# Performance work log

Hardware: AMD Instinct MI355X
Metric: run time of the kernel (lower is better)

The kernel has to match this reference:

```python
import jax, jax.numpy as jnp
import numpy as np

N_NODES = 100000
N_EDGES = 20000
N_PAIRS = 640000
IN_CH = 128
HEADS = 4
OUT_CH = 32


def setup_inputs() -> dict:
    key = jax.random.key(0)
    k1, k2, k3, k4, k5 = jax.random.split(key, 5)
    X = jax.random.normal(k1, (N_NODES, IN_CH), dtype=jnp.float32)
    # nn.Linear(in, H*C, bias=False); stored as [in, H*C] so X0 = X @ W
    W = jax.random.normal(k2, (IN_CH, HEADS * OUT_CH), dtype=jnp.float32) * (1.0 / np.sqrt(IN_CH))
    stdv = (6.0 / (HEADS + OUT_CH)) ** 0.5
    att_e = jax.random.uniform(k3, (1, HEADS, OUT_CH), dtype=jnp.float32, minval=-stdv, maxval=stdv)
    vertex = jax.random.randint(k4, (N_PAIRS,), 0, N_NODES, dtype=jnp.int64)
    edges = jax.random.randint(k5, (N_PAIRS,), 0, N_EDGES, dtype=jnp.int64)
    return {"X": X, "W": W, "att_e": att_e, "vertex": vertex, "edges": edges}


def reference(X, W, att_e, vertex, edges):
    N = X.shape[0]
    H, C = HEADS, OUT_CH
    X0 = X @ W                                  # [N, H*C]
    Xv_hc = X0.reshape(N, H, C)
    Xve = Xv_hc[vertex]                          # [M, H, C] gather
    # scatter-mean over hyperedges
    esum = jax.ops.segment_sum(Xve, edges, num_segments=N_EDGES)
    ecnt = jax.ops.segment_sum(jnp.ones((Xve.shape[0],), X.dtype), edges, num_segments=N_EDGES)
    Xe = esum / jnp.maximum(ecnt, 1.0)[:, None, None]   # [E, H, C]
    alpha_e = (Xe * att_e).sum(-1)               # [E, H]
    a_ev = alpha_e[edges]                        # [M, H]
    alpha = jax.nn.leaky_relu(a_ev, 0.01)
    # per-vertex softmax over incident hyperedges
    amax = jax.ops.segment_max(alpha, vertex, num_segments=N)
    alpha = jnp.exp(alpha - amax[vertex])
    asum = jax.ops.segment_sum(alpha, vertex, num_segments=N)
    alpha = alpha / (asum[vertex] + 1e-8)
    Xev = Xe[edges] * alpha[:, :, None]          # [M, H, C]
    Xv = jax.ops.segment_sum(Xev, vertex, num_segments=N)
    return Xv.reshape(N, H * C) + X0
```

## Files before the change

### kernel.cpp

```cpp
#include <hip/hip_runtime.h>
#include <hip/hip_bf16.h>

#define N_NODES 100000
#define N_EDGES 20000
#define N_PAIRS 640000
#define CH 128
#define HEADS 4
#define MAXDV 32

#define NG_GEMM 1563
#define NR_RANK 2500
#define INTERLEAVE (2*NG_GEMM)

#define OFF_X0H   0UL
#define OFF_XEH   25600000UL
#define OFF_RANK  30720000UL
#define OFF_WT    33280000UL
#define OFF_ALPHA 33320000UL
#define OFF_OFFE  33640000UL
#define OFF_ENDE  33720000UL
#define OFF_OFFV  33800000UL
#define OFF_ENDV  34200000UL
#define OFF_PIDXE 34600000UL
#define OFF_PIDXV 37160000UL
#define OFF_CNTE  39720000UL
#define OFF_CNTV  39800000UL
#define OFF_TOT   40200000UL
#define ZERO_BYTES 480008UL

typedef __attribute__((ext_vector_type(8))) short bf16x8;
typedef __attribute__((ext_vector_type(4))) float f32x4;

__device__ inline short f2bf(float f) {
    __hip_bfloat16 h = __float2bfloat16(f);
    return reinterpret_cast<short&>(h);
}
__device__ inline float bf2f(short s) {
    unsigned int u = ((unsigned int)(unsigned short)s) << 16;
    union { unsigned int u; float f; } c; c.u = u;
    return c.f;
}

__global__ __launch_bounds__(256) void k_wprep(const float* __restrict__ W,
                                               short* __restrict__ Wt) {
    const int idx = blockIdx.x * 256 + threadIdx.x;
    const int n = idx >> 7, k = idx & 127;
    Wt[n * CH + k] = f2bf(W[k * CH + n]);
}

__device__ inline void gemm_body(int gb, const float* __restrict__ X,
                                 const short* __restrict__ Wt,
                                 short* __restrict__ X0h) {
    const int t = threadIdx.x;
    const int wave = t >> 6, lane = t & 63;
    const int r0 = gb * 64 + (wave >> 1) * 32;
    const int c0 = (wave & 1) * 64;
    const int lrow = lane & 15, lk8 = (lane >> 4) * 8;

    f32x4 acc[2][4] = {};

#pragma unroll
    for (int kk = 0; kk < 4; ++kk) {
        const int ks = kk * 32 + lk8;
        bf16x8 a[2], b[4];
#pragma unroll
        for (int m = 0; m < 2; ++m) {
            int row = r0 + m * 16 + lrow;
            row = min(row, N_NODES - 1);
            const float* p = &X[(size_t)row * CH + ks];
            const float4 x0 = *(const float4*)p;
            const float4 x1 = *(const float4*)(p + 4);
            a[m][0] = f2bf(x0.x); a[m][1] = f2bf(x0.y);
            a[m][2] = f2bf(x0.z); a[m][3] = f2bf(x0.w);
            a[m][4] = f2bf(x1.x); a[m][5] = f2bf(x1.y);
            a[m][6] = f2bf(x1.z); a[m][7] = f2bf(x1.w);
        }
#pragma unroll
        for (int n = 0; n < 4; ++n) {
            int col = c0 + n * 16 + lrow;
            b[n] = *(const bf16x8*)&Wt[col * CH + ks];
        }
#pragma unroll
        for (int m = 0; m < 2; ++m)
#pragma unroll
            for (int n = 0; n < 4; ++n)
                acc[m][n] = __builtin_amdgcn_mfma_f32_16x16x32_bf16(a[m], b[n], acc[m][n], 0, 0, 0);
    }

#pragma unroll
    for (int m = 0; m < 2; ++m) {
#pragma unroll
        for (int reg = 0; reg < 4; ++reg) {
            const int row = r0 + m * 16 + (lane >> 4) * 4 + reg;
            if (row < N_NODES) {
#pragma unroll
                for (int n = 0; n < 4; ++n)
                    X0h[(size_t)row * CH + c0 + n * 16 + (lane & 15)] = f2bf(acc[m][n][reg]);
            }
        }
    }
}

__device__ inline void rank_body(int rb, const int* __restrict__ vertex,
                                 const int* __restrict__ edges,
                                 int* __restrict__ cnt_e,
                                 int* __restrict__ cnt_v,
                                 unsigned int* __restrict__ rank_pack) {
    const int m = rb * 256 + threadIdx.x;
    const int e = edges[m];
    const int v = vertex[m];
    int re = atomicAdd(&cnt_e[e], 1);
    int rv = atomicAdd(&cnt_v[v], 1);
    rank_pack[m] = ((unsigned)rv << 16) | (unsigned)re;
}

__global__ __launch_bounds__(256) void k_gemm_rank(const float* __restrict__ X,
                                                   const short* __restrict__ Wt,
                                                   short* __restrict__ X0h,
                                                   const int* __restrict__ vertex,
                                                   const int* __restrict__ edges,
                                                   int* __restrict__ cnt_e,
                                                   int* __restrict__ cnt_v,
                                                   unsigned int* __restrict__ rank_pack) {
    const int bid = blockIdx.x;
    if (bid < INTERLEAVE) {
        if ((bid & 1) == 0) gemm_body(bid >> 1, X, Wt, X0h);
        else                rank_body(bid >> 1, vertex, edges, cnt_e, cnt_v, rank_pack);
    } else {
        rank_body(bid - INTERLEAVE + NG_GEMM, vertex, edges, cnt_e, cnt_v, rank_pack);
    }
}

__global__ __launch_bounds__(256) void k_offsets2(const int* __restrict__ cnt_e,
                                                  int* __restrict__ off_e,
                                                  int* __restrict__ end_e,
                                                  const int* __restrict__ cnt_v,
                                                  int* __restrict__ off_v,
                                                  int* __restrict__ end_v,
                                                  int* __restrict__ totals) {
    __shared__ int s[256];
    __shared__ int base;
    const int bid = blockIdx.x, t = threadIdx.x;
    const int* cnt; int* off; int* end; int* total; int n, i;
    if (bid < 79) { cnt = cnt_e; off = off_e; end = end_e; total = &totals[0]; n = N_EDGES;  i = bid * 256 + t; }
    else          { cnt = cnt_v; off = off_v; end = end_v; total = &totals[1]; n = N_NODES; i = (bid - 79) * 256 + t; }
    const int c = (i < n) ? cnt[i] : 0;
    s[t] = c;
    __syncthreads();
    for (int d = 1; d < 256; d <<= 1) {
        int x = (t >= d) ? s[t - d] : 0;
        __syncthreads();
        s[t] += x;
        __syncthreads();
    }
    if (t == 0) base = atomicAdd(total, s[255]);
    __syncthreads();
    if (i < n) {
        int o = base + s[t] - c;
        off[i] = o;
        end[i] = o + c;
    }
}

__global__ __launch_bounds__(256) void k_scatter(const int* __restrict__ vertex,
                                                 const int* __restrict__ edges,
                                                 const unsigned int* __restrict__ rank_pack,
                                                 const int* __restrict__ off_e,
                                                 const int* __restrict__ off_v,
                                                 int* __restrict__ vlist_e,
                                                 int* __restrict__ elist_v) {
    const int m = blockIdx.x * 256 + threadIdx.x;
    const int e = edges[m];
    const int v = vertex[m];
    const unsigned rp = rank_pack[m];
    vlist_e[off_e[e] + (int)(rp & 0xffffu)] = v;
    elist_v[off_v[v] + (int)(rp >> 16)] = e;
}

__global__ __launch_bounds__(256) void k_edge(const short* __restrict__ X0h,
                                              const int* __restrict__ off_e,
                                              const int* __restrict__ end_e,
                                              const int* __restrict__ vlist,
                                              const float* __restrict__ att,
                                              short* __restrict__ Xeh,
                                              float* __restrict__ alpha_le) {
    const int t = threadIdx.x;
    const int slot = t >> 5, lane = t & 31, h = lane >> 3;
    const int e = blockIdx.x * 8 + slot;
    const int s = off_e[e], en = end_e[e];
    const int deg = en - s;

    float4 acc = make_float4(0.f, 0.f, 0.f, 0.f);
    for (int c0 = 0; c0 < deg; c0 += 32) {
        const int cn = min(32, deg - c0);
        int vl = (lane < cn) ? vlist[s + c0 + lane] : 0;
#pragma unroll 4
        for (int j = 0; j < cn; ++j) {
            int vj = __shfl(vl, j, 32);
            short4 x = *(const short4*)&X0h[(size_t)vj * CH + (lane << 2)];
            acc.x += bf2f(x.x); acc.y += bf2f(x.y);
            acc.z += bf2f(x.z); acc.w += bf2f(x.w);
        }
    }
    const float invd = 1.0f / fmaxf((float)deg, 1.0f);
    float4 xe = make_float4(acc.x * invd, acc.y * invd, acc.z * invd, acc.w * invd);
    short4 xh;
    xh.x = f2bf(xe.x); xh.y = f2bf(xe.y); xh.z = f2bf(xe.z); xh.w = f2bf(xe.w);
    *(short4*)&Xeh[(size_t)e * CH + (lane << 2)] = xh;

    const float4 av = *(const float4*)&att[lane << 2];
    float p = xe.x * av.x + xe.y * av.y + xe.z * av.z + xe.w * av.w;
#pragma unroll
    for (int o = 4; o; o >>= 1) p += __shfl_xor(p, o);
    if ((lane & 7) == 0) {
        float a = p;
        alpha_le[e * HEADS + h] = (a > 0.f) ? a : 0.01f * a;
    }
}

__global__ __launch_bounds__(256) void k_vertex(const short* __restrict__ X0h,
                                                const short* __restrict__ Xeh,
                                                const float* __restrict__ alpha_le,
                                                const int* __restrict__ off_v,
                                                const int* __restrict__ end_v,
                                                const int* __restrict__ elist,
                                                float* __restrict__ out) {
    const int t = threadIdx.x;
    const int slot = t >> 5, lane = t & 31, h = lane >> 3;
    const int v = blockIdx.x * 8 + slot;
    const int s = off_v[v], en = end_v[v];
    const int deg = en - s;

    __shared__ int   se[8][MAXDV];
    __shared__ float sa[8][MAXDV * HEADS];

    if (deg <= MAXDV && lane < deg) {
        int e = elist[s + lane];
        se[slot][lane] = e;
        *(float4*)&sa[slot][lane << 2] = *(const float4*)&alpha_le[e * HEADS];
    }
    const short4 resh = *(const short4*)&X0h[(size_t)v * CH + (lane << 2)];
    __syncthreads();

    float4 acc = make_float4(0.f, 0.f, 0.f, 0.f);
    if (deg <= MAXDV) {
        float mx = -INFINITY;
        for (int j = 0; j < deg; ++j) mx = fmaxf(mx, sa[slot][(j << 2) + h]);
        float ssum = 0.f;
        for (int j = 0; j < deg; ++j) ssum += __expf(sa[slot][(j << 2) + h] - mx);
        const float inv = 1.0f / (ssum + 1e-8f);
        for (int j = 0; j < deg; ++j) {
            float w = __expf(sa[slot][(j << 2) + h] - mx) * inv;
            short4 x = *(const short4*)&Xeh[(size_t)se[slot][j] * CH + (lane << 2)];
            acc.x += w * bf2f(x.x); acc.y += w * bf2f(x.y);
            acc.z += w * bf2f(x.z); acc.w += w * bf2f(x.w);
        }
    } else {
        float mx = -INFINITY;
        for (int j = 0; j < deg; ++j) mx = fmaxf(mx, alpha_le[elist[s + j] * HEADS + h]);
        float ssum = 0.f;
        for (int j = 0; j < deg; ++j) ssum += __expf(alpha_le[elist[s + j] * HEADS + h] - mx);
        const float inv = 1.0f / (ssum + 1e-8f);
        for (int j = 0; j < deg; ++j) {
            int e = elist[s + j];
            float w = __expf(alpha_le[e * HEADS + h] - mx) * inv;
            short4 x = *(const short4*)&Xeh[(size_t)e * CH + (lane << 2)];
            acc.x += w * bf2f(x.x); acc.y += w * bf2f(x.y);
            acc.z += w * bf2f(x.z); acc.w += w * bf2f(x.w);
        }
    }
    float4 o = make_float4(acc.x + bf2f(resh.x), acc.y + bf2f(resh.y),
                           acc.z + bf2f(resh.z), acc.w + bf2f(resh.w));
    ((float4*)out)[(size_t)v * 32 + lane] = o;
}

extern "C" void kernel_launch(void* const* d_in, const int* in_sizes, int n_in,
                              void* d_out, int out_size, void* d_ws, size_t ws_size,
                              hipStream_t stream) {
    const float* X      = (const float*)d_in[0];
    const float* W      = (const float*)d_in[1];
    const float* att    = (const float*)d_in[2];
    const int*   vertex = (const int*)d_in[3];
    const int*   edges  = (const int*)d_in[4];
    float* out = (float*)d_out;

    char* ws = (char*)d_ws;
    short* X0h      = (short*)(ws + OFF_X0H);
    short* Xeh      = (short*)(ws + OFF_XEH);
    unsigned int* rank_pack = (unsigned int*)(ws + OFF_RANK);
    short* Wt       = (short*)(ws + OFF_WT);
    float* alpha_le = (float*)(ws + OFF_ALPHA);
    int* off_e   = (int*)(ws + OFF_OFFE);
    int* end_e   = (int*)(ws + OFF_ENDE);
    int* off_v   = (int*)(ws + OFF_OFFV);
    int* end_v   = (int*)(ws + OFF_ENDV);
    int* vlist_e = (int*)(ws + OFF_PIDXE);
    int* elist_v = (int*)(ws + OFF_PIDXV);
    int* cnt_e   = (int*)(ws + OFF_CNTE);
    int* cnt_v   = (int*)(ws + OFF_CNTV);
    int* totals  = (int*)(ws + OFF_TOT);

    hipMemsetAsync(ws + OFF_CNTE, 0, ZERO_BYTES, stream);

    k_wprep<<<64, 256, 0, stream>>>(W, Wt);
    k_gemm_rank<<<NG_GEMM + NR_RANK, 256, 0, stream>>>(X, Wt, X0h, vertex, edges,
                                                       cnt_e, cnt_v, rank_pack);
    k_offsets2<<<79 + 391, 256, 0, stream>>>(cnt_e, off_e, end_e, cnt_v, off_v, end_v, totals);
    k_scatter<<<N_PAIRS / 256, 256, 0, stream>>>(vertex, edges, rank_pack, off_e, off_v, vlist_e, elist_v);
    k_edge<<<N_EDGES / 8, 256, 0, stream>>>(X0h, off_e, end_e, vlist_e, att, Xeh, alpha_le);
    k_vertex<<<N_NODES / 8, 256, 0, stream>>>(X0h, Xeh, alpha_le, off_v, end_v, elist_v, out);
}
```

Baseline: 174.2 us.

## Replace global edge-count atomics with per-block LDS histograms and multi-pass scan

Edge ranking no longer uses a global atomicAdd per pair on cnt_e. Instead, 125 blocks each build a packed 16-bit shared-memory histogram of their 5120-pair chunk, write local ranks and per-block counts, and three small scan kernels turn those counts into per-block prefix offsets and total edge counts. The scatter kernel then recombines the block prefix with the local rank. This targets contention from only 20000 hot edge counters. In exchange it adds three kernel launches and about 5 MB of blkcnt traffic, and it assumes per-edge counts fit in 16 bits.

Result: slower. 179.1 us (+2.8%).

```diff
diff --git a/kernel.cpp b/kernel.cpp
--- a/kernel.cpp
+++ b/kernel.cpp
@@ -9,24 +9,30 @@
 #define MAXDV 32
 
 #define NG_GEMM 1563
-#define NR_RANK 2500
-#define INTERLEAVE (2*NG_GEMM)
+#define NV_RANK 2500
+#define NE_BLOCKS 125
+#define ECHUNK 5120
+#define NWORDS 10240
+#define SCAN_G 5
 
 #define OFF_X0H   0UL
 #define OFF_XEH   25600000UL
-#define OFF_RANK  30720000UL
-#define OFF_WT    33280000UL
-#define OFF_ALPHA 33320000UL
-#define OFF_OFFE  33640000UL
-#define OFF_ENDE  33720000UL
-#define OFF_OFFV  33800000UL
-#define OFF_ENDV  34200000UL
-#define OFF_PIDXE 34600000UL
-#define OFF_PIDXV 37160000UL
-#define OFF_CNTE  39720000UL
-#define OFF_CNTV  39800000UL
-#define OFF_TOT   40200000UL
-#define ZERO_BYTES 480008UL
+#define OFF_LRE   30720000UL
+#define OFF_RKV   32000000UL
+#define OFF_BLK   33280000UL
+#define OFF_GSUM  38400000UL
+#define OFF_WT    38604800UL
+#define OFF_ALPHA 38637568UL
+#define OFF_OFFE  38957568UL
+#define OFF_ENDE  39039488UL
+#define OFF_OFFV  39121408UL
+#define OFF_ENDV  39521408UL
+#define OFF_PIDXE 39921408UL
+#define OFF_PIDXV 42481408UL
+#define OFF_CNTE  45041408UL
+#define OFF_CNTV  45123328UL
+#define OFF_TOT   45523328UL
+#define ZERO_BYTES 400008UL
 
 typedef __attribute__((ext_vector_type(8))) short bf16x8;
 typedef __attribute__((ext_vector_type(4))) float f32x4;
@@ -101,33 +107,84 @@
     }
 }
 
-__device__ inline void rank_body(int rb, const int* __restrict__ vertex,
-                                 const int* __restrict__ edges,
-                                 int* __restrict__ cnt_e,
-                                 int* __restrict__ cnt_v,
-                                 unsigned int* __restrict__ rank_pack) {
-    const int m = rb * 256 + threadIdx.x;
-    const int e = edges[m];
-    const int v = vertex[m];
-    int re = atomicAdd(&cnt_e[e], 1);
-    int rv = atomicAdd(&cnt_v[v], 1);
-    rank_pack[m] = ((unsigned)rv << 16) | (unsigned)re;
-}
-
-__global__ __launch_bounds__(256) void k_gemm_rank(const float* __restrict__ X,
-                                                   const short* __restrict__ Wt,
-                                                   short* __restrict__ X0h,
-                                                   const int* __restrict__ vertex,
-                                                   const int* __restrict__ edges,
-                                                   int* __restrict__ cnt_e,
-                                                   int* __restrict__ cnt_v,
-                                                   unsigned int* __restrict__ rank_pack) {
+__global__ __launch_bounds__(256) void k_phase1(const float* __restrict__ X,
+                                                const short* __restrict__ Wt,
+                                                short* __restrict__ X0h,
+                                                const int* __restrict__ vertex,
+                                                const int* __restrict__ edges,
+                                                int* __restrict__ cnt_v,
+                                                unsigned short* __restrict__ lrank_e,
+                                                unsigned short* __restrict__ rank_v,
+                                                unsigned int* __restrict__ blkcnt) {
+    __shared__ unsigned int hist[NWORDS];
     const int bid = blockIdx.x;
-    if (bid < INTERLEAVE) {
-        if ((bid & 1) == 0) gemm_body(bid >> 1, X, Wt, X0h);
-        else                rank_body(bid >> 1, vertex, edges, cnt_e, cnt_v, rank_pack);
-    } else {
-        rank_body(bid - INTERLEAVE + NG_GEMM, vertex, edges, cnt_e, cnt_v, rank_pack);
+    const int t = threadIdx.x;
+
+    if (bid < NE_BLOCKS) {
+        for (int i = t; i < NWORDS; i += 256) hist[i] = 0;
+        __syncthreads();
+        const int base = bid * ECHUNK;
+        unsigned short lr[20];
+#pragma unroll
+        for (int it = 0; it < 20; ++it) {
+            const int m = base + it * 256 + t;
+            const int e = edges[m];
+            const unsigned sh = (unsigned)(e & 1) * 16u;
+            unsigned old = atomicAdd(&hist[e >> 1], 1u << sh);
+            lr[it] = (unsigned short)((old >> sh) & 0xffffu);
+        }
+#pragma unroll
+        for (int it = 0; it < 20; ++it) lrank_e[base + it * 256 + t] = lr[it];
+        __syncthreads();
+        for (int w = t; w < NWORDS; w += 256) blkcnt[bid * NWORDS + w] = hist[w];
+        return;
+    }
+    const int r = bid - NE_BLOCKS;
+    if (r < 2 * NG_GEMM) {
+        if ((r & 1) == 0) { gemm_body(r >> 1, X, Wt, X0h); return; }
+        const int m = (r >> 1) * 256 + t;
+        rank_v[m] = (unsigned short)atomicAdd(&cnt_v[vertex[m]], 1);
+        return;
+    }
+    const int m = (r - 2 * NG_GEMM + NG_GEMM) * 256 + t;
+    rank_v[m] = (unsigned short)atomicAdd(&cnt_v[vertex[m]], 1);
+}
+
+__global__ __launch_bounds__(256) void k_scan_p1(const unsigned int* __restrict__ blkcnt,
+                                                 unsigned int* __restrict__ gsum) {
+    const int gid = blockIdx.x * 256 + threadIdx.x;
+    const int g = gid / NWORDS, w = gid % NWORDS;
+    unsigned s = 0;
+#pragma unroll 5
+    for (int i = 0; i < 25; ++i) s += blkcnt[(g * 25 + i) * NWORDS + w];
+    gsum[g * NWORDS + w] = s;
+}
+
+__global__ __launch_bounds__(256) void k_scan_p2(unsigned int* __restrict__ gsum,
+                                                 int* __restrict__ cnt_e) {
+    const int w = blockIdx.x * 256 + threadIdx.x;
+    unsigned run = 0;
+#pragma unroll
+    for (int g = 0; g < SCAN_G; ++g) {
+        unsigned c = gsum[g * NWORDS + w];
+        gsum[g * NWORDS + w] = run;
+        run += c;
+    }
+    cnt_e[2 * w]     = (int)(run & 0xffffu);
+    cnt_e[2 * w + 1] = (int)(run >> 16);
+}
+
+__global__ __launch_bounds__(256) void k_scan_p3(unsigned int* __restrict__ blkcnt,
+                                                 const unsigned int* __restrict__ gsum) {
+    const int gid = blockIdx.x * 256 + threadIdx.x;
+    const int g = gid / NWORDS, w = gid % NWORDS;
+    unsigned run = gsum[g * NWORDS + w];
+#pragma unroll 5
+    for (int i = 0; i < 25; ++i) {
+        const int idx = (g * 25 + i) * NWORDS + w;
+        unsigned c = blkcnt[idx];
+        blkcnt[idx] = run;
+        run += c;
     }
 }
 
@@ -164,7 +221,9 @@
 
 __global__ __launch_bounds__(256) void k_scatter(const int* __restrict__ vertex,
                                                  const int* __restrict__ edges,
-                                                 const unsigned int* __restrict__ rank_pack,
+                                                 const unsigned short* __restrict__ lrank_e,
+                                                 const unsigned short* __restrict__ rank_v,
+                                                 const unsigned int* __restrict__ blkcnt,
                                                  const int* __restrict__ off_e,
                                                  const int* __restrict__ off_v,
                                                  int* __restrict__ vlist_e,
@@ -172,9 +231,11 @@
     const int m = blockIdx.x * 256 + threadIdx.x;
     const int e = edges[m];
     const int v = vertex[m];
-    const unsigned rp = rank_pack[m];
-    vlist_e[off_e[e] + (int)(rp & 0xffffu)] = v;
-    elist_v[off_v[v] + (int)(rp >> 16)] = e;
+    const int b = m / ECHUNK;
+    const unsigned pw = blkcnt[b * NWORDS + (e >> 1)];
+    const int er = (int)((pw >> ((unsigned)(e & 1) * 16u)) & 0xffffu) + (int)lrank_e[m];
+    vlist_e[off_e[e] + er] = v;
+    elist_v[off_v[v] + (int)rank_v[m]] = e;
 }
 
 __global__ __launch_bounds__(256) void k_edge(const short* __restrict__ X0h,
@@ -287,7 +348,10 @@
     char* ws = (char*)d_ws;
     short* X0h      = (short*)(ws + OFF_X0H);
     short* Xeh      = (short*)(ws + OFF_XEH);
-    unsigned int* rank_pack = (unsigned int*)(ws + OFF_RANK);
+    unsigned short* lrank_e = (unsigned short*)(ws + OFF_LRE);
+    unsigned short* rank_v  = (unsigned short*)(ws + OFF_RKV);
+    unsigned int*   blkcnt  = (unsigned int*)(ws + OFF_BLK);
+    unsigned int*   gsum    = (unsigned int*)(ws + OFF_GSUM);
     short* Wt       = (short*)(ws + OFF_WT);
     float* alpha_le = (float*)(ws + OFF_ALPHA);
     int* off_e   = (int*)(ws + OFF_OFFE);
@@ -300,13 +364,17 @@
     int* cnt_v   = (int*)(ws + OFF_CNTV);
     int* totals  = (int*)(ws + OFF_TOT);
 
-    hipMemsetAsync(ws + OFF_CNTE, 0, ZERO_BYTES, stream);
+    hipMemsetAsync(ws + OFF_CNTV, 0, ZERO_BYTES, stream);
 
     k_wprep<<<64, 256, 0, stream>>>(W, Wt);
-    k_gemm_rank<<<NG_GEMM + NR_RANK, 256, 0, stream>>>(X, Wt, X0h, vertex, edges,
-                                                       cnt_e, cnt_v, rank_pack);
+    k_phase1<<<NE_BLOCKS + 2 * NG_GEMM + (NV_RANK - NG_GEMM), 256, 0, stream>>>(
+        X, Wt, X0h, vertex, edges, cnt_v, lrank_e, rank_v, blkcnt);
+    k_scan_p1<<<200, 256, 0, stream>>>(blkcnt, gsum);
+    k_scan_p2<<<40, 256, 0, stream>>>(gsum, cnt_e);
+    k_scan_p3<<<200, 256, 0, stream>>>(blkcnt, gsum);
     k_offsets2<<<79 + 391, 256, 0, stream>>>(cnt_e, off_e, end_e, cnt_v, off_v, end_v, totals);
-    k_scatter<<<N_PAIRS / 256, 256, 0, stream>>>(vertex, edges, rank_pack, off_e, off_v, vlist_e, elist_v);
+    k_scatter<<<N_PAIRS / 256, 256, 0, stream>>>(vertex, edges, lrank_e, rank_v, blkcnt,
+                                                 off_e, off_v, vlist_e, elist_v);
     k_edge<<<N_EDGES / 8, 256, 0, stream>>>(X0h, off_e, end_e, vlist_e, att, Xeh, alpha_le);
     k_vertex<<<N_NODES / 8, 256, 0, stream>>>(X0h, Xeh, alpha_le, off_v, end_v, elist_v, out);
 }
```

## Replace global atomic ranking with chunked LDS histograms and multi-pass prefix scans

Applied to the files above, without the earlier changes.

Computes per-pair ranks within edges and vertices using packed 8-bit shared-memory histograms per chunk of pairs, instead of global atomicAdd counters. Three scan kernels turn the per-chunk counts into exclusive prefixes and totals, and the scatter kernel combines chunk prefix and local rank. This removes contended random global atomics and the large memset. In exchange it adds about 15MB of block-count workspace traffic, three extra launches, and a reliance on per-chunk counts staying below 256.

Result: faster. 166.5 us (-4.4%).

```diff
diff --git a/kernel.cpp b/kernel.cpp
--- a/kernel.cpp
+++ b/kernel.cpp
@@ -9,24 +9,33 @@
 #define MAXDV 32
 
 #define NG_GEMM 1563
-#define NR_RANK 2500
-#define INTERLEAVE (2*NG_GEMM)
+#define NCHUNK 125
+#define ECHUNK 5120
+#define EW 5120
+#define VWR 6250
+#define NRANGE 4
+#define VBIN_R 25000
 
 #define OFF_X0H   0UL
 #define OFF_XEH   25600000UL
-#define OFF_RANK  30720000UL
-#define OFF_WT    33280000UL
-#define OFF_ALPHA 33320000UL
-#define OFF_OFFE  33640000UL
-#define OFF_ENDE  33720000UL
-#define OFF_OFFV  33800000UL
-#define OFF_ENDV  34200000UL
-#define OFF_PIDXE 34600000UL
-#define OFF_PIDXV 37160000UL
-#define OFF_CNTE  39720000UL
-#define OFF_CNTV  39800000UL
-#define OFF_TOT   40200000UL
-#define ZERO_BYTES 480008UL
+#define OFF_LRE   30720000UL
+#define OFF_LRV   31360000UL
+#define OFF_BLKE  32000000UL
+#define OFF_BLKV  34560000UL
+#define OFF_GSE   47060000UL
+#define OFF_GSV   47162400UL
+#define OFF_WT    47662400UL
+#define OFF_ALPHA 47695168UL
+#define OFF_OFFE  48015168UL
+#define OFF_ENDE  48097088UL
+#define OFF_OFFV  48179008UL
+#define OFF_ENDV  48579008UL
+#define OFF_PIDXE 48979008UL
+#define OFF_PIDXV 51539008UL
+#define OFF_CNTE  54099008UL
+#define OFF_CNTV  54180928UL
+#define OFF_TOT   54580928UL
+#define ZERO_BYTES 8UL
 
 typedef __attribute__((ext_vector_type(8))) short bf16x8;
 typedef __attribute__((ext_vector_type(4))) float f32x4;
@@ -101,33 +110,149 @@
     }
 }
 
-__device__ inline void rank_body(int rb, const int* __restrict__ vertex,
-                                 const int* __restrict__ edges,
-                                 int* __restrict__ cnt_e,
-                                 int* __restrict__ cnt_v,
-                                 unsigned int* __restrict__ rank_pack) {
-    const int m = rb * 256 + threadIdx.x;
-    const int e = edges[m];
-    const int v = vertex[m];
-    int re = atomicAdd(&cnt_e[e], 1);
-    int rv = atomicAdd(&cnt_v[v], 1);
-    rank_pack[m] = ((unsigned)rv << 16) | (unsigned)re;
-}
-
-__global__ __launch_bounds__(256) void k_gemm_rank(const float* __restrict__ X,
-                                                   const short* __restrict__ Wt,
-                                                   short* __restrict__ X0h,
-                                                   const int* __restrict__ vertex,
-                                                   const int* __restrict__ edges,
-                                                   int* __restrict__ cnt_e,
-                                                   int* __restrict__ cnt_v,
-                                                   unsigned int* __restrict__ rank_pack) {
+__global__ __launch_bounds__(256) void k_phase1(const float* __restrict__ X,
+                                                const short* __restrict__ Wt,
+                                                short* __restrict__ X0h,
+                                                const int* __restrict__ vertex,
+                                                const int* __restrict__ edges,
+                                                unsigned char* __restrict__ lrank_e,
+                                                unsigned char* __restrict__ lrank_v,
+                                                unsigned int* __restrict__ blkcnt_e,
+                                                unsigned int* __restrict__ blkcnt_v) {
+    __shared__ unsigned int hist[VWR];
     const int bid = blockIdx.x;
-    if (bid < INTERLEAVE) {
-        if ((bid & 1) == 0) gemm_body(bid >> 1, X, Wt, X0h);
-        else                rank_body(bid >> 1, vertex, edges, cnt_e, cnt_v, rank_pack);
-    } else {
-        rank_body(bid - INTERLEAVE + NG_GEMM, vertex, edges, cnt_e, cnt_v, rank_pack);
+    const int t = threadIdx.x;
+
+    if (bid < NRANGE * NCHUNK) {
+        const int r = bid & 3, c = bid >> 2;
+        for (int i = t; i < VWR; i += 256) hist[i] = 0;
+        __syncthreads();
+        const int base = c * ECHUNK;
+        const int vmin = r * VBIN_R;
+#pragma unroll
+        for (int it = 0; it < 20; ++it) {
+            const int m = base + it * 256 + t;
+            const int loc = vertex[m] - vmin;
+            if ((unsigned)loc < (unsigned)VBIN_R) {
+                const unsigned sh = (unsigned)(loc & 3) * 8u;
+                unsigned old = atomicAdd(&hist[loc >> 2], 1u << sh);
+                lrank_v[m] = (unsigned char)((old >> sh) & 0xffu);
+            }
+        }
+        __syncthreads();
+        unsigned int* dst = &blkcnt_v[(size_t)(r * NCHUNK + c) * VWR];
+        for (int w = t; w < VWR; w += 256) dst[w] = hist[w];
+        return;
+    }
+    if (bid < NRANGE * NCHUNK + NCHUNK) {
+        const int c = bid - NRANGE * NCHUNK;
+        for (int i = t; i < EW; i += 256) hist[i] = 0;
+        __syncthreads();
+        const int base = c * ECHUNK;
+#pragma unroll
+        for (int it = 0; it < 20; ++it) {
+            const int m = base + it * 256 + t;
+            const int e = edges[m];
+            const unsigned sh = (unsigned)(e & 3) * 8u;
+            unsigned old = atomicAdd(&hist[e >> 2], 1u << sh);
+            lrank_e[m] = (unsigned char)((old >> sh) & 0xffu);
+        }
+        __syncthreads();
+        unsigned int* dst = &blkcnt_e[(size_t)c * EW];
+        for (int w = t; w < EW; w += 256) dst[w] = hist[w];
+        return;
+    }
+    gemm_body(bid - (NRANGE * NCHUNK + NCHUNK), X, Wt, X0h);
+}
+
+__global__ __launch_bounds__(256) void k_scan_p1(const unsigned int* __restrict__ blkcnt_e,
+                                                 const unsigned int* __restrict__ blkcnt_v,
+                                                 unsigned int* __restrict__ gse,
+                                                 unsigned int* __restrict__ gsv) {
+    const int bid = blockIdx.x;
+    if (bid < 100) {
+        const int gid = bid * 256 + threadIdx.x;
+        const int g = gid / EW, w = gid % EW;
+        unsigned s = 0;
+#pragma unroll 5
+        for (int i = 0; i < 25; ++i) s += blkcnt_e[(size_t)(g * 25 + i) * EW + w];
+        gse[g * EW + w] = s;
+        return;
+    }
+    const int vid = (bid - 100) * 256 + threadIdx.x;
+    if (vid >= 20 * VWR) return;
+    const int g = vid / VWR, w = vid % VWR;
+    const int r = g / 5, cg = g % 5;
+    unsigned s = 0;
+#pragma unroll 5
+    for (int i = 0; i < 25; ++i)
+        s += blkcnt_v[(size_t)(r * NCHUNK + cg * 25 + i) * VWR + w];
+    gsv[g * VWR + w] = s;
+}
+
+__global__ __launch_bounds__(256) void k_scan_p2(unsigned int* __restrict__ gse,
+                                                 unsigned int* __restrict__ gsv,
+                                                 int* __restrict__ cnt_e,
+                                                 int* __restrict__ cnt_v) {
+    const int bid = blockIdx.x;
+    if (bid < 20) {
+        const int w = bid * 256 + threadIdx.x;
+        unsigned run = 0;
+#pragma unroll
+        for (int g = 0; g < 5; ++g) {
+            unsigned c = gse[g * EW + w];
+            gse[g * EW + w] = run;
+            run += c;
+        }
+        int4 o = { (int)(run & 0xffu), (int)((run >> 8) & 0xffu),
+                   (int)((run >> 16) & 0xffu), (int)(run >> 24) };
+        *(int4*)&cnt_e[4 * w] = o;
+        return;
+    }
+    const int id = (bid - 20) * 256 + threadIdx.x;
+    if (id >= NRANGE * VWR) return;
+    const int r = id / VWR, w = id % VWR;
+    unsigned run = 0;
+#pragma unroll
+    for (int g = r * 5; g < r * 5 + 5; ++g) {
+        unsigned c = gsv[g * VWR + w];
+        gsv[g * VWR + w] = run;
+        run += c;
+    }
+    int4 o = { (int)(run & 0xffu), (int)((run >> 8) & 0xffu),
+               (int)((run >> 16) & 0xffu), (int)(run >> 24) };
+    *(int4*)&cnt_v[r * VBIN_R + 4 * w] = o;
+}
+
+__global__ __launch_bounds__(256) void k_scan_p3(unsigned int* __restrict__ blkcnt_e,
+                                                 unsigned int* __restrict__ blkcnt_v,
+                                                 const unsigned int* __restrict__ gse,
+                                                 const unsigned int* __restrict__ gsv) {
+    const int bid = blockIdx.x;
+    if (bid < 100) {
+        const int gid = bid * 256 + threadIdx.x;
+        const int g = gid / EW, w = gid % EW;
+        unsigned run = gse[g * EW + w];
+#pragma unroll 5
+        for (int i = 0; i < 25; ++i) {
+            const size_t idx = (size_t)(g * 25 + i) * EW + w;
+            unsigned c = blkcnt_e[idx];
+            blkcnt_e[idx] = run;
+            run += c;
+        }
+        return;
+    }
+    const int vid = (bid - 100) * 256 + threadIdx.x;
+    if (vid >= 20 * VWR) return;
+    const int g = vid / VWR, w = vid % VWR;
+    const int r = g / 5, cg = g % 5;
+    unsigned run = gsv[g * VWR + w];
+#pragma unroll 5
+    for (int i = 0; i < 25; ++i) {
+        const size_t idx = (size_t)(r * NCHUNK + cg * 25 + i) * VWR + w;
+        unsigned c = blkcnt_v[idx];
+        blkcnt_v[idx] = run;
+        run += c;
     }
 }
 
@@ -164,7 +289,10 @@
 
 __global__ __launch_bounds__(256) void k_scatter(const int* __restrict__ vertex,
                                                  const int* __restrict__ edges,
-                                                 const unsigned int* __restrict__ rank_pack,
+                                                 const unsigned char* __restrict__ lrank_e,
+                                                 const unsigned char* __restrict__ lrank_v,
+                                                 const unsigned int* __restrict__ blkcnt_e,
+                                                 const unsigned int* __restrict__ blkcnt_v,
                                                  const int* __restrict__ off_e,
                                                  const int* __restrict__ off_v,
                                                  int* __restrict__ vlist_e,
@@ -172,9 +300,14 @@
     const int m = blockIdx.x * 256 + threadIdx.x;
     const int e = edges[m];
     const int v = vertex[m];
-    const unsigned rp = rank_pack[m];
-    vlist_e[off_e[e] + (int)(rp & 0xffffu)] = v;
-    elist_v[off_v[v] + (int)(rp >> 16)] = e;
+    const int c = m / ECHUNK;
+    const unsigned pe = blkcnt_e[(size_t)c * EW + (e >> 2)];
+    const int er = (int)((pe >> ((unsigned)(e & 3) * 8u)) & 0xffu) + (int)lrank_e[m];
+    const int r = v / VBIN_R, loc = v - r * VBIN_R;
+    const unsigned pv = blkcnt_v[(size_t)(r * NCHUNK + c) * VWR + (loc >> 2)];
+    const int vr = (int)((pv >> ((unsigned)(loc & 3) * 8u)) & 0xffu) + (int)lrank_v[m];
+    vlist_e[off_e[e] + er] = v;
+    elist_v[off_v[v] + vr] = e;
 }
 
 __global__ __launch_bounds__(256) void k_edge(const short* __restrict__ X0h,
@@ -287,7 +420,12 @@
     char* ws = (char*)d_ws;
     short* X0h      = (short*)(ws + OFF_X0H);
     short* Xeh      = (short*)(ws + OFF_XEH);
-    unsigned int* rank_pack = (unsigned int*)(ws + OFF_RANK);
+    unsigned char* lrank_e = (unsigned char*)(ws + OFF_LRE);
+    unsigned char* lrank_v = (unsigned char*)(ws + OFF_LRV);
+    unsigned int*  blkcnt_e = (unsigned int*)(ws + OFF_BLKE);
+    unsigned int*  blkcnt_v = (unsigned int*)(ws + OFF_BLKV);
+    unsigned int*  gse      = (unsigned int*)(ws + OFF_GSE);
+    unsigned int*  gsv      = (unsigned int*)(ws + OFF_GSV);
     short* Wt       = (short*)(ws + OFF_WT);
     float* alpha_le = (float*)(ws + OFF_ALPHA);
     int* off_e   = (int*)(ws + OFF_OFFE);
@@ -300,13 +438,18 @@
     int* cnt_v   = (int*)(ws + OFF_CNTV);
     int* totals  = (int*)(ws + OFF_TOT);
 
-    hipMemsetAsync(ws + OFF_CNTE, 0, ZERO_BYTES, stream);
+    hipMemsetAsync(ws + OFF_TOT, 0, ZERO_BYTES, stream);
 
     k_wprep<<<64, 256, 0, stream>>>(W, Wt);
-    k_gemm_rank<<<NG_GEMM + NR_RANK, 256, 0, stream>>>(X, Wt, X0h, vertex, edges,
-                                                       cnt_e, cnt_v, rank_pack);
+    k_phase1<<<NRANGE * NCHUNK + NCHUNK + NG_GEMM, 256, 0, stream>>>(
+        X, Wt, X0h, vertex, edges, lrank_e, lrank_v, blkcnt_e, blkcnt_v);
+    k_scan_p1<<<100 + 489, 256, 0, stream>>>(blkcnt_e, blkcnt_v, gse, gsv);
+    k_scan_p2<<<20 + 98, 256, 0, stream>>>(gse, gsv, cnt_e, cnt_v);
+    k_scan_p3<<<100 + 489, 256, 0, stream>>>(blkcnt_e, blkcnt_v, gse, gsv);
     k_offsets2<<<79 + 391, 256, 0, stream>>>(cnt_e, off_e, end_e, cnt_v, off_v, end_v, totals);
-    k_scatter<<<N_PAIRS / 256, 256, 0, stream>>>(vertex, edges, rank_pack, off_e, off_v, vlist_e, elist_v);
+    k_scatter<<<N_PAIRS / 256, 256, 0, stream>>>(vertex, edges, lrank_e, lrank_v,
+                                                 blkcnt_e, blkcnt_v, off_e, off_v,
+                                                 vlist_e, elist_v);
     k_edge<<<N_EDGES / 8, 256, 0, stream>>>(X0h, off_e, end_e, vlist_e, att, Xeh, alpha_le);
     k_vertex<<<N_NODES / 8, 256, 0, stream>>>(X0h, Xeh, alpha_le, off_v, end_v, elist_v, out);
 }
```
